# Performance work log

Measured on AMD Instinct MI355X. Metric: run time of the kernel, lower is better.

The kernel has to match this reference:

```python
import jax, jax.numpy as jnp
import numpy as np

NUM_GROUPS = 32
EPS = 1e-6
HEAD = 8


def group_norm(x, gamma, beta):
    # x: (b, c, h, w); normalize per group of channels over (c/g, h, w)
    b, c, h, w = x.shape
    g = NUM_GROUPS
    xg = x.reshape(b, g, c // g, h, w)
    mean = xg.mean(axis=(2, 3, 4), keepdims=True)
    var = xg.var(axis=(2, 3, 4), keepdims=True)
    xn = ((xg - mean) * jax.lax.rsqrt(var + EPS)).reshape(b, c, h, w)
    return xn * gamma[None, :, None, None] + beta[None, :, None, None]


def setup_inputs() -> dict:
    key = jax.random.key(0)
    ks = jax.random.split(key, 6)
    b, c, h, w = 8, 512, 64, 64
    sd = 1.0 / np.sqrt(c)
    return {
        "x": jax.random.normal(ks[0], (b, c, h, w), jnp.float32),
        "gamma": jnp.ones((c,), jnp.float32),
        "beta": jnp.zeros((c,), jnp.float32),
        "Wq": jax.random.normal(ks[1], (c, c), jnp.float32) * sd,
        "Wk": jax.random.normal(ks[2], (c, c), jnp.float32) * sd,
        "Wv": jax.random.normal(ks[3], (c, c), jnp.float32) * sd,
        "Wp": jax.random.normal(ks[4], (c, c), jnp.float32) * sd,
        "bp": jnp.zeros((c,), jnp.float32),
    }


def reference(x, gamma, beta, Wq, Wk, Wv, Wp, bp):
    b, c, h, w = x.shape
    hd = c // HEAD
    scale = jnp.sqrt(jnp.float32(hd))  # NOTE: original MULTIPLIES by sqrt(d)
    xn = group_norm(x, gamma, beta)            # (b, c, h, w)
    x_ = xn.reshape(b, c, h * w).transpose(0, 2, 1)  # (b, n, c), n = h*w
    # torch Linear: y = x @ W.T
    Q = (x_ @ Wq.T).reshape(b, h * w, HEAD, hd)
    K = (x_ @ Wk.T).reshape(b, h * w, HEAD, hd)
    V = (x_ @ Wv.T).reshape(b, h * w, HEAD, hd)
    # einsum 'bhid,bhjd->bhij' with axes (b, n, head, hd): per-position head gram
    dots = jnp.einsum('bnid,bnjd->bnij', Q, K) * scale  # (b, n, head, head)
    att = jax.nn.softmax(dots, axis=1)  # softmax over the SPATIAL axis (dim=1)
    out = jnp.einsum('bnij,bnjd->bnid', att, V).reshape(b, h * w, c)
    out = out @ Wp.T + bp  # dropout is identity at inference
    return out.transpose(0, 2, 1).reshape(b, c, h, w) + xn  # residual adds normed x
```

## Files before the change

kernel.cpp:

```cpp
#include <hip/hip_runtime.h>
#include <stdint.h>

typedef unsigned short ushort_t;
typedef _Float16 half8 __attribute__((ext_vector_type(8)));
typedef float f32x4 __attribute__((ext_vector_type(4)));

#define GLOBAL_AS __attribute__((address_space(1)))
#define LDS_AS    __attribute__((address_space(3)))

__device__ __forceinline__ float bf2f(ushort_t u) {
    union { unsigned i; float f; } v; v.i = ((unsigned)u) << 16; return v.f;
}
__device__ __forceinline__ ushort_t f2h(float f) {
    union { _Float16 h; ushort_t u; } v; v.h = (_Float16)f; return v.u;
}
__device__ __forceinline__ float h2f(ushort_t u) {
    union { _Float16 h; ushort_t u; } v; v.u = u; return (float)v.h;
}

__device__ __forceinline__ void async16(const void* g, void* l) {
    __builtin_amdgcn_global_load_lds((const GLOBAL_AS uint32_t*)g,
                                     (LDS_AS uint32_t*)l, 16, 0, 0);
}

__device__ __forceinline__ int is_bf16_in(const uint32_t* g32) {
    return *g32 == 0x3F803F80u;
}

__global__ __launch_bounds__(256) void prep(const void* Wq, const void* Wk,
                                            const void* Wv, const void* Wp,
                                            const void* g, const void* be, const void* bp,
                                            ushort_t* Wh, float* gcan, float* bcan,
                                            float* bpcan, const uint32_t* g32) {
    const int id = blockIdx.x;
    const int isbf = is_bf16_in(g32);
    if (id < 512) {
        const int wsel = id >> 7, wblk = id & 127;
        const void* src = (wsel == 0) ? Wq : (wsel == 1) ? Wk : (wsel == 2) ? Wv : Wp;
        ushort_t* dst = Wh + (size_t)wsel * 262144;
        const int e0 = wblk * 2048 + threadIdx.x * 8;
        ushort_t o[8];
        if (isbf) {
            uint4 u = *(const uint4*)((const ushort_t*)src + e0);
            const ushort_t* e = (const ushort_t*)&u;
#pragma unroll
            for (int j = 0; j < 8; ++j) o[j] = f2h(bf2f(e[j]));
        } else {
            float4 a = *(const float4*)((const float*)src + e0);
            float4 b = *(const float4*)((const float*)src + e0 + 4);
            o[0] = f2h(a.x); o[1] = f2h(a.y); o[2] = f2h(a.z); o[3] = f2h(a.w);
            o[4] = f2h(b.x); o[5] = f2h(b.y); o[6] = f2h(b.z); o[7] = f2h(b.w);
        }
        *(uint4*)(dst + e0) = *(const uint4*)o;
    } else {
        int t = threadIdx.x + (id - 512) * 256;
        if (isbf) {
            gcan[t]  = bf2f(((const ushort_t*)g)[t]);
            bcan[t]  = bf2f(((const ushort_t*)be)[t]);
            bpcan[t] = bf2f(((const ushort_t*)bp)[t]);
        } else {
            gcan[t]  = ((const float*)g)[t];
            bcan[t]  = ((const float*)be)[t];
            bpcan[t] = ((const float*)bp)[t];
        }
    }
}

__global__ __launch_bounds__(256) void gn_part(const void* xv, float* __restrict__ psums,
                                               const uint32_t* g32) {
    const int bx = blockIdx.x, t = threadIdx.x;
    const size_t base = (size_t)(bx >> 3) * 65536 + (size_t)(bx & 7) * 8192;
    float s = 0.f, sq = 0.f;
    if (is_bf16_in(g32)) {
        const ushort_t* p = (const ushort_t*)xv + base;
        for (int i = 0; i < 4; ++i) {
            uint4 u = ((const uint4*)p)[t + 256 * i];
            const ushort_t* e = (const ushort_t*)&u;
#pragma unroll
            for (int j = 0; j < 8; ++j) { float f = bf2f(e[j]); s += f; sq += f * f; }
        }
    } else {
        const float* p = (const float*)xv + base;
        for (int i = 0; i < 8; ++i) {
            float4 v = ((const float4*)p)[t + 256 * i];
            s += v.x + v.y + v.z + v.w;
            sq += v.x * v.x + v.y * v.y + v.z * v.z + v.w * v.w;
        }
    }
    __shared__ float ls[256], lq[256];
    ls[t] = s; lq[t] = sq;
    __syncthreads();
    for (int off = 128; off > 0; off >>= 1) {
        if (t < off) { ls[t] += ls[t + off]; lq[t] += lq[t + off]; }
        __syncthreads();
    }
    if (t == 0) { psums[bx * 2] = ls[0]; psums[bx * 2 + 1] = lq[0]; }
}

__global__ __launch_bounds__(256) void gn_apply_t(const void* xv,
                                                  const float* __restrict__ gcan,
                                                  const float* __restrict__ bcan,
                                                  const float* __restrict__ psums,
                                                  ushort_t* __restrict__ xnt,
                                                  ushort_t* __restrict__ xnc,
                                                  const uint32_t* g32) {
    const int nt = blockIdx.x;
    const int ct = blockIdx.y;
    const int b  = blockIdx.z;
    const int t  = threadIdx.x;
    const int c0 = ct * 64, n0 = nt * 64;
    __shared__ __align__(16) ushort_t tile[64 * 80];
    __shared__ float scS[64], shS[64];
    if (t < 64) {
        int c = c0 + t;
        int g = c >> 4;
        float s = 0.f, q = 0.f;
#pragma unroll
        for (int k = 0; k < 8; ++k) {
            s += psums[((b * 32 + g) * 8 + k) * 2];
            q += psums[((b * 32 + g) * 8 + k) * 2 + 1];
        }
        float mean = s * (1.f / 65536.f);
        float var  = q * (1.f / 65536.f) - mean * mean;
        float rstd = rsqrtf(fmaxf(var, 0.f) + 1e-6f);
        float sc = rstd * gcan[c];
        scS[t] = sc;
        shS[t] = bcan[c] - mean * sc;
    }
    __syncthreads();
    if (is_bf16_in(g32)) {
        const ushort_t* x = (const ushort_t*)xv;
#pragma unroll
        for (int p = 0; p < 2; ++p) {
            int u = p * 256 + t;
            int cc = u >> 3, nc = u & 7;
            int c = c0 + cc;
            size_t gidx = ((size_t)(b * 512 + c)) * 4096 + n0 + nc * 8;
            uint4 raw = *(const uint4*)(x + gidx);
            float sc = scS[cc], sh = shS[cc];
            const ushort_t* e = (const ushort_t*)&raw;
            ushort_t hv[8];
#pragma unroll
            for (int j = 0; j < 8; ++j) {
                hv[j] = f2h(bf2f(e[j]) * sc + sh);
                tile[(nc * 8 + j) * 80 + cc] = hv[j];
            }
            *(uint4*)(xnc + gidx) = *(const uint4*)hv;
        }
    } else {
        const float* x = (const float*)xv;
#pragma unroll
        for (int p = 0; p < 4; ++p) {
            int u = p * 256 + t;
            int cc = u >> 4, nc = u & 15;
            int c = c0 + cc;
            size_t gidx = ((size_t)(b * 512 + c)) * 4096 + n0 + nc * 4;
            float4 raw = *(const float4*)(x + gidx);
            float sc = scS[cc], sh = shS[cc];
            ushort_t hv[4];
            hv[0] = f2h(raw.x * sc + sh);
            hv[1] = f2h(raw.y * sc + sh);
            hv[2] = f2h(raw.z * sc + sh);
            hv[3] = f2h(raw.w * sc + sh);
#pragma unroll
            for (int j = 0; j < 4; ++j) tile[(nc * 4 + j) * 80 + cc] = hv[j];
            *(uint2*)(xnc + gidx) = *(const uint2*)hv;
        }
    }
    __syncthreads();
#pragma unroll
    for (int p = 0; p < 2; ++p) {
        int u = p * 256 + t;
        int nn = u >> 3, cchunk = u & 7;
        uint4 o = *(const uint4*)(tile + nn * 80 + cchunk * 8);
        *(uint4*)(xnt + ((size_t)(b * 4096 + n0 + nn)) * 512 + c0 + cchunk * 8) = o;
    }
}

__device__ __forceinline__ void gemm256_core(const ushort_t* __restrict__ A,
                                             const ushort_t* __restrict__ Bm,
                                             int m0, int n0, f32x4 acc[8][4]) {
    __shared__ __align__(16) ushort_t lds[2][4][8192];
    const int t = threadIdx.x;
    const int l = t & 63, w = t >> 6;
    const int wmi = w >> 2, wni = w & 3;
    const int lr = l & 15, q = l >> 4;
    const int rxor = lr & 7;
    const int sr = t >> 3;
    const int sc = (t & 7) ^ (sr & 7);

    f32x4 zero = {0.f, 0.f, 0.f, 0.f};
#pragma unroll
    for (int mf = 0; mf < 8; ++mf)
#pragma unroll
        for (int nf = 0; nf < 4; ++nf) acc[mf][nf] = zero;

    auto stage = [&](int kt, int h) {
        const ushort_t* src = ((h < 2) ? A + (size_t)(m0 + h * 128 + sr) * 512
                                       : Bm + (size_t)(n0 + (h - 2) * 128 + sr) * 512)
                              + kt * 64 + sc * 8;
        ushort_t* dst = &lds[kt & 1][h][w * 512];
        async16(src, dst);
        async16(src + 64 * 512, dst + 4096);
    };

    stage(0, 0); stage(0, 1); stage(0, 2); stage(0, 3);
    stage(1, 2); stage(1, 3);
    asm volatile("s_waitcnt vmcnt(4)" ::: "memory");
    __builtin_amdgcn_s_barrier();

    half8 bfr[4][2];
    for (int kt = 0; kt < 8; ++kt) {
        const ushort_t* Ah = &lds[kt & 1][wmi][0];
        const ushort_t* Bh = &lds[kt & 1][2 + (wni >> 1)][(wni & 1) * 4096];
#pragma unroll
        for (int p = 0; p < 4; ++p) {
            half8 afr[2][2];
#pragma unroll
            for (int i = 0; i < 2; ++i)
#pragma unroll
                for (int kh = 0; kh < 2; ++kh)
                    afr[i][kh] = *(const half8*)(Ah + (2 * p + i) * 1024 + lr * 64 +
                                                 (((kh << 2) | q) ^ rxor) * 8);
            if (p == 0) {
#pragma unroll
                for (int nf = 0; nf < 4; ++nf)
#pragma unroll
                    for (int kh = 0; kh < 2; ++kh)
                        bfr[nf][kh] = *(const half8*)(Bh + nf * 1024 + lr * 64 +
                                                      (((kh << 2) | q) ^ rxor) * 8);
            }
            if (p < 2) { if (kt + 1 < 8) stage(kt + 1, p); }
            else       { if (kt + 2 < 8) stage(kt + 2, p); }
            __builtin_amdgcn_s_barrier();
            asm volatile("s_waitcnt lgkmcnt(0)" ::: "memory");
            __builtin_amdgcn_sched_barrier(0);
            __builtin_amdgcn_s_setprio(1);
#pragma unroll
            for (int i = 0; i < 2; ++i)
#pragma unroll
                for (int nf = 0; nf < 4; ++nf) {
                    acc[2 * p + i][nf] = __builtin_amdgcn_mfma_f32_16x16x32_f16(
                        afr[i][0], bfr[nf][0], acc[2 * p + i][nf], 0, 0, 0);
                    acc[2 * p + i][nf] = __builtin_amdgcn_mfma_f32_16x16x32_f16(
                        afr[i][1], bfr[nf][1], acc[2 * p + i][nf], 0, 0, 0);
                }
            __builtin_amdgcn_s_setprio(0);
            __builtin_amdgcn_s_barrier();
        }
        if (kt < 7) {
            if (kt < 6) asm volatile("s_waitcnt vmcnt(4)" ::: "memory");
            else        asm volatile("s_waitcnt vmcnt(0)" ::: "memory");
            __builtin_amdgcn_s_barrier();
        }
    }
}

__global__ __launch_bounds__(512, 2) void gemm_qkv(const ushort_t* __restrict__ xnt,
                                                   const ushort_t* __restrict__ Wh,
                                                   ushort_t* __restrict__ Qo,
                                                   ushort_t* __restrict__ Ko,
                                                   ushort_t* __restrict__ Vo) {
    const int id = blockIdx.x;
    const int xcd = id & 7, s = id >> 3;
    const int mloc = s / 6, r = s % 6;
    const int m0 = (xcd * 16 + mloc) * 256;
    const int n0 = (r & 1) * 256;
    const int z  = r >> 1;
    const ushort_t* B = Wh + (size_t)z * 262144;
    ushort_t* C = (z == 0) ? Qo : (z == 1) ? Ko : Vo;
    f32x4 acc[8][4];
    gemm256_core(xnt, B, m0, n0, acc);
    const int t = threadIdx.x, l = t & 63, w = t >> 6;
    const int wmi = w >> 2, wni = w & 3;
    const int lr = l & 15, q = l >> 4;
#pragma unroll
    for (int mf = 0; mf < 8; ++mf)
#pragma unroll
        for (int nf = 0; nf < 4; ++nf)
#pragma unroll
            for (int rr = 0; rr < 4; ++rr) {
                int row = m0 + wmi * 128 + mf * 16 + q * 4 + rr;
                int cc  = n0 + wni * 64 + nf * 16 + lr;
                C[(size_t)row * 512 + cc] = f2h(acc[mf][nf][rr]);
            }
}

__global__ __launch_bounds__(256) void dots_smax(const ushort_t* __restrict__ Q,
                                                 const ushort_t* __restrict__ K,
                                                 float* __restrict__ dots,
                                                 float* __restrict__ pmax,
                                                 float* __restrict__ psum) {
    const int chunk = blockIdx.x;
    const int t = threadIdx.x, l = t & 63, w = t >> 6;
    const int m = l & 15, q = l >> 4, col = m;
    __shared__ float sd[128][64];
    __shared__ float lm[4][64], lsum[4][64];
#pragma unroll
    for (int i = 0; i < 16; ++i) {
        int gpl = (i * 4 + w) * 2;
        int gp0 = chunk * 128 + gpl;
        const size_t base = (size_t)(gp0 + (m >> 3)) * 512 + (m & 7) * 64 + q * 8;
        half8 a0 = *(const half8*)(Q + base);
        half8 a1 = *(const half8*)(Q + base + 32);
        half8 b0 = *(const half8*)(K + base);
        half8 b1 = *(const half8*)(K + base + 32);
        f32x4 acc = {0.f, 0.f, 0.f, 0.f};
        acc = __builtin_amdgcn_mfma_f32_16x16x32_f16(a0, b0, acc, 0, 0, 0);
        acc = __builtin_amdgcn_mfma_f32_16x16x32_f16(a1, b1, acc, 0, 0, 0);
#pragma unroll
        for (int r = 0; r < 4; ++r) {
            int row = q * 4 + r;
            if (row < 8 && col < 8) {
                float v = acc[r] * 8.0f;
                int ij = row * 8 + col;
                sd[gpl][ij] = v;
                dots[(size_t)(gp0)*64 + ij] = v;
            }
            if (row >= 8 && col >= 8) {
                float v = acc[r] * 8.0f;
                int ij = (row - 8) * 8 + (col - 8);
                sd[gpl + 1][ij] = v;
                dots[(size_t)(gp0 + 1) * 64 + ij] = v;
            }
        }
    }
    __syncthreads();
    const int ij = l;
    float mx = -1e30f;
    float v[32];
#pragma unroll
    for (int r = 0; r < 32; ++r) { v[r] = sd[w * 32 + r][ij]; mx = fmaxf(mx, v[r]); }
    lm[w][ij] = mx;
    __syncthreads();
    float cm = fmaxf(fmaxf(lm[0][ij], lm[1][ij]), fmaxf(lm[2][ij], lm[3][ij]));
    float sum = 0.f;
#pragma unroll
    for (int r = 0; r < 32; ++r) sum += __expf(v[r] - cm);
    lsum[w][ij] = sum;
    __syncthreads();
    if (w == 0) {
        pmax[chunk * 64 + ij] = cm;
        psum[chunk * 64 + ij] = lsum[0][ij] + lsum[1][ij] + lsum[2][ij] + lsum[3][ij];
    }
}

__global__ __launch_bounds__(256) void attn_apply(const float* __restrict__ dots,
                                                  const float* __restrict__ pmax,
                                                  const float* __restrict__ psum,
                                                  const ushort_t* __restrict__ V,
                                                  ushort_t* __restrict__ P) {
    const int t = threadIdx.x, l = t & 63, w = t >> 6;
    const int gp_base = blockIdx.x * 16;
    const int b = gp_base >> 12;
    __shared__ float pm4[4][64], ps4[4][64];
    __shared__ float Mv[64], Siv[64];
    {
        const int cg = w * 8;
        float m = -1e30f;
        float pmv[8], psv[8];
#pragma unroll
        for (int c = 0; c < 8; ++c) {
            pmv[c] = pmax[(b * 32 + cg + c) * 64 + l];
            psv[c] = psum[(b * 32 + cg + c) * 64 + l];
            m = fmaxf(m, pmv[c]);
        }
        float s = 0.f;
#pragma unroll
        for (int c = 0; c < 8; ++c) s += psv[c] * __expf(pmv[c] - m);
        pm4[w][l] = m; ps4[w][l] = s;
    }
    __syncthreads();
    if (w == 0) {
        float M = fmaxf(fmaxf(pm4[0][l], pm4[1][l]), fmaxf(pm4[2][l], pm4[3][l]));
        float S = ps4[0][l] * __expf(pm4[0][l] - M) + ps4[1][l] * __expf(pm4[1][l] - M)
                + ps4[2][l] * __expf(pm4[2][l] - M) + ps4[3][l] * __expf(pm4[3][l] - M);
        Mv[l] = M;
        Siv[l] = 1.f / S;
    }
    __syncthreads();
    const float mv = Mv[l], siv = Siv[l];
    __shared__ float att[4][64];
    __shared__ __align__(16) ushort_t vb[4][512];
    const int i = l >> 3, dc = l & 7;
    for (int p = 0; p < 4; ++p) {
        int gp = gp_base + w * 4 + p;
        float d = dots[(size_t)gp * 64 + l];
        att[w][l] = __expf(d - mv) * siv;
        *(uint4*)(&vb[w][l * 8]) = *(const uint4*)(V + (size_t)gp * 512 + l * 8);
        float o[8] = {0, 0, 0, 0, 0, 0, 0, 0};
#pragma unroll
        for (int j = 0; j < 8; ++j) {
            float a = att[w][i * 8 + j];
            uint4 vv = *(const uint4*)(&vb[w][j * 64 + dc * 8]);
            const ushort_t* ve = (const ushort_t*)&vv;
#pragma unroll
            for (int k2 = 0; k2 < 8; ++k2) o[k2] += a * h2f(ve[k2]);
        }
        ushort_t ou[8];
#pragma unroll
        for (int k2 = 0; k2 < 8; ++k2) ou[k2] = f2h(o[k2]);
        *(uint4*)(P + (size_t)gp * 512 + l * 8) = *(const uint4*)ou;
    }
}

__global__ __launch_bounds__(512, 2) void gemm_out(const ushort_t* __restrict__ Wph,
                                                   const ushort_t* __restrict__ P,
                                                   const ushort_t* __restrict__ xnc,
                                                   const float* __restrict__ bpcan,
                                                   float* __restrict__ out) {
    const int id = blockIdx.x;
    const int b  = id & 7;
    const int s  = id >> 3;
    const int o0 = (s & 1) * 256;
    const int n1 = (s >> 1) * 256;
    f32x4 acc[8][4];
    gemm256_core(Wph, P + (size_t)b * 4096 * 512, o0, n1, acc);
    const int t = threadIdx.x, l = t & 63, w = t >> 6;
    const int wmi = w >> 2, wni = w & 3;
    const int lr = l & 15, q = l >> 4;
#pragma unroll
    for (int mf = 0; mf < 8; ++mf) {
#pragma unroll
        for (int rr = 0; rr < 4; ++rr) {
            int o = o0 + wmi * 128 + mf * 16 + q * 4 + rr;
            float bias = bpcan[o];
#pragma unroll
            for (int nf = 0; nf < 4; ++nf) {
                int n = n1 + wni * 64 + nf * 16 + lr;
                size_t idx = ((size_t)(b * 512 + o)) * 4096 + n;
                out[idx] = acc[mf][nf][rr] + bias + h2f(xnc[idx]);
            }
        }
    }
}

extern "C" void kernel_launch(void* const* d_in, const int* in_sizes, int n_in,
                              void* d_out, int out_size, void* d_ws, size_t ws_size,
                              hipStream_t stream) {
    const void* x     = d_in[0];
    const void* gamma = d_in[1];
    const void* beta  = d_in[2];
    const void* Wq    = d_in[3];
    const void* Wk    = d_in[4];
    const void* Wv    = d_in[5];
    const void* Wp    = d_in[6];
    const void* bp    = d_in[7];
    const uint32_t* g32 = (const uint32_t*)gamma;
    float* out = (float*)d_out;

    char* ws = (char*)d_ws;
    const size_t SZ = 33554432;
    ushort_t* xnt = (ushort_t*)(ws);
    ushort_t* Qh  = (ushort_t*)(ws + 1 * SZ);
    ushort_t* Kh  = (ushort_t*)(ws + 2 * SZ);
    ushort_t* Vh  = (ushort_t*)(ws + 3 * SZ);
    float* dots   = (float*)(ws + 4 * SZ);
    ushort_t* Wh  = (ushort_t*)(ws + 4 * SZ + 8388608);
    ushort_t* xnc = (ushort_t*)(ws + 4 * SZ + 8388608 + 2097152);
    char* tail    = ws + 4 * SZ + 8388608 + 2097152 + SZ;
    float* gcan   = (float*)(tail);
    float* bcan   = gcan + 512;
    float* bpcan  = bcan + 512;
    float* psums  = bpcan + 512;
    float* pmax   = psums + 4096;
    float* psumS  = pmax + 16384;
    ushort_t* Pb  = xnt;

    prep      <<<514, 256, 0, stream>>>(Wq, Wk, Wv, Wp, gamma, beta, bp,
                                        Wh, gcan, bcan, bpcan, g32);
    gn_part   <<<2048, 256, 0, stream>>>(x, psums, g32);
    gn_apply_t<<<dim3(64, 8, 8), 256, 0, stream>>>(x, gcan, bcan, psums, xnt, xnc, g32);
    gemm_qkv  <<<768, 512, 0, stream>>>(xnt, Wh, Qh, Kh, Vh);
    dots_smax <<<256, 256, 0, stream>>>(Qh, Kh, dots, pmax, psumS);
    attn_apply<<<2048, 256, 0, stream>>>(dots, pmax, psumS, Vh, Pb);
    gemm_out  <<<256, 512, 0, stream>>>(Wh + 3 * 262144, Pb, xnc, bpcan, out);
}
```

Measured before the change: 267.8 us.

## Software-pipeline LDS fragment loads against MFMA in QKV GEMM core

Restructures the GEMM inner loop so A fragments for the next sub-tile are read from LDS while the current sub-tile's MFMAs run, using double-buffered register fragments (cur/nxt). Global and LDS address arithmetic is precomputed outside the loop into base pointers. Each phase now has one barrier instead of two, which shortens sync time. The cost is higher register pressure from the extra fragment buffers, and there is some risk around the ordering of barriers against the async stage writes.

```diff
diff --git a/kernel.cpp b/kernel.cpp
--- a/kernel.cpp
+++ b/kernel.cpp
@@ -22,6 +22,9 @@
     __builtin_amdgcn_global_load_lds((const GLOBAL_AS uint32_t*)g,
                                      (LDS_AS uint32_t*)l, 16, 0, 0);
 }
+
+#define LGKM0_SB do { asm volatile("s_waitcnt lgkmcnt(0)" ::: "memory"); \
+                      __builtin_amdgcn_sched_barrier(0); } while (0)
 
 __device__ __forceinline__ int is_bf16_in(const uint32_t* g32) {
     return *g32 == 0x3F803F80u;
@@ -189,68 +192,126 @@
     const int sr = t >> 3;
     const int sc = (t & 7) ^ (sr & 7);
 
+    const ushort_t* gA0 = A  + (size_t)(m0 + sr) * 512 + sc * 8;
+    const ushort_t* gA1 = A  + (size_t)(m0 + 128 + sr) * 512 + sc * 8;
+    const ushort_t* gB0 = Bm + (size_t)(n0 + sr) * 512 + sc * 8;
+    const ushort_t* gB1 = Bm + (size_t)(n0 + 128 + sr) * 512 + sc * 8;
+
+    const int cK0 = (q ^ rxor) * 8;
+    const int cK1 = ((4 | q) ^ rxor) * 8;
+    const ushort_t* lbase = &lds[0][0][0];
+    const ushort_t* pA0 = lbase + wmi * 8192 + lr * 64 + cK0;
+    const ushort_t* pA1 = lbase + wmi * 8192 + lr * 64 + cK1;
+    const ushort_t* pB0 = lbase + (2 + (wni >> 1)) * 8192 + (wni & 1) * 4096 + lr * 64 + cK0;
+    const ushort_t* pB1 = lbase + (2 + (wni >> 1)) * 8192 + (wni & 1) * 4096 + lr * 64 + cK1;
+
+    auto stg = [&](const ushort_t* gp, int kt, int h) {
+        ushort_t* d = (ushort_t*)(&lds[0][0][0]) + (kt & 1) * 32768 + h * 8192 + w * 512;
+        async16(gp + kt * 64, d);
+        async16(gp + kt * 64 + 64 * 512, d + 4096);
+    };
+
     f32x4 zero = {0.f, 0.f, 0.f, 0.f};
 #pragma unroll
     for (int mf = 0; mf < 8; ++mf)
 #pragma unroll
         for (int nf = 0; nf < 4; ++nf) acc[mf][nf] = zero;
 
-    auto stage = [&](int kt, int h) {
-        const ushort_t* src = ((h < 2) ? A + (size_t)(m0 + h * 128 + sr) * 512
-                                       : Bm + (size_t)(n0 + (h - 2) * 128 + sr) * 512)
-                              + kt * 64 + sc * 8;
-        ushort_t* dst = &lds[kt & 1][h][w * 512];
-        async16(src, dst);
-        async16(src + 64 * 512, dst + 4096);
-    };
-
-    stage(0, 0); stage(0, 1); stage(0, 2); stage(0, 3);
-    stage(1, 2); stage(1, 3);
+    stg(gA0, 0, 0); stg(gA1, 0, 1); stg(gB0, 0, 2); stg(gB1, 0, 3);
+    stg(gB0, 1, 2); stg(gB1, 1, 3);
     asm volatile("s_waitcnt vmcnt(4)" ::: "memory");
     __builtin_amdgcn_s_barrier();
 
-    half8 bfr[4][2];
     for (int kt = 0; kt < 8; ++kt) {
-        const ushort_t* Ah = &lds[kt & 1][wmi][0];
-        const ushort_t* Bh = &lds[kt & 1][2 + (wni >> 1)][(wni & 1) * 4096];
-#pragma unroll
-        for (int p = 0; p < 4; ++p) {
-            half8 afr[2][2];
-#pragma unroll
-            for (int i = 0; i < 2; ++i)
-#pragma unroll
-                for (int kh = 0; kh < 2; ++kh)
-                    afr[i][kh] = *(const half8*)(Ah + (2 * p + i) * 1024 + lr * 64 +
-                                                 (((kh << 2) | q) ^ rxor) * 8);
-            if (p == 0) {
-#pragma unroll
-                for (int nf = 0; nf < 4; ++nf)
-#pragma unroll
-                    for (int kh = 0; kh < 2; ++kh)
-                        bfr[nf][kh] = *(const half8*)(Bh + nf * 1024 + lr * 64 +
-                                                      (((kh << 2) | q) ^ rxor) * 8);
-            }
-            if (p < 2) { if (kt + 1 < 8) stage(kt + 1, p); }
-            else       { if (kt + 2 < 8) stage(kt + 2, p); }
-            __builtin_amdgcn_s_barrier();
-            asm volatile("s_waitcnt lgkmcnt(0)" ::: "memory");
-            __builtin_amdgcn_sched_barrier(0);
-            __builtin_amdgcn_s_setprio(1);
-#pragma unroll
-            for (int i = 0; i < 2; ++i)
-#pragma unroll
-                for (int nf = 0; nf < 4; ++nf) {
-                    acc[2 * p + i][nf] = __builtin_amdgcn_mfma_f32_16x16x32_f16(
-                        afr[i][0], bfr[nf][0], acc[2 * p + i][nf], 0, 0, 0);
-                    acc[2 * p + i][nf] = __builtin_amdgcn_mfma_f32_16x16x32_f16(
-                        afr[i][1], bfr[nf][1], acc[2 * p + i][nf], 0, 0, 0);
-                }
-            __builtin_amdgcn_s_setprio(0);
-            __builtin_amdgcn_s_barrier();
-        }
-        if (kt < 7) {
-            if (kt < 6) asm volatile("s_waitcnt vmcnt(4)" ::: "memory");
-            else        asm volatile("s_waitcnt vmcnt(0)" ::: "memory");
+        const int bo = (kt & 1) << 15;
+        const ushort_t* a0 = pA0 + bo;
+        const ushort_t* a1 = pA1 + bo;
+        const ushort_t* b0 = pB0 + bo;
+        const ushort_t* b1 = pB1 + bo;
+        half8 bfr[4][2], cur[2][2], nxt[2][2];
+#pragma unroll
+        for (int nf = 0; nf < 4; ++nf) {
+            bfr[nf][0] = *(const half8*)(b0 + nf * 1024);
+            bfr[nf][1] = *(const half8*)(b1 + nf * 1024);
+        }
+#pragma unroll
+        for (int i = 0; i < 2; ++i) {
+            cur[i][0] = *(const half8*)(a0 + i * 1024);
+            cur[i][1] = *(const half8*)(a1 + i * 1024);
+        }
+        if (kt + 1 < 8) stg(gA0, kt + 1, 0);
+        LGKM0_SB;
+#pragma unroll
+        for (int i = 0; i < 2; ++i) {
+            nxt[i][0] = *(const half8*)(a0 + (2 + i) * 1024);
+            nxt[i][1] = *(const half8*)(a1 + (2 + i) * 1024);
+        }
+        if (kt + 1 < 8) stg(gA1, kt + 1, 1);
+        __builtin_amdgcn_s_setprio(1);
+#pragma unroll
+        for (int i = 0; i < 2; ++i)
+#pragma unroll
+            for (int nf = 0; nf < 4; ++nf) {
+                acc[i][nf] = __builtin_amdgcn_mfma_f32_16x16x32_f16(
+                    cur[i][0], bfr[nf][0], acc[i][nf], 0, 0, 0);
+                acc[i][nf] = __builtin_amdgcn_mfma_f32_16x16x32_f16(
+                    cur[i][1], bfr[nf][1], acc[i][nf], 0, 0, 0);
+            }
+        __builtin_amdgcn_s_setprio(0);
+        __builtin_amdgcn_s_barrier();
+        LGKM0_SB;
+#pragma unroll
+        for (int i = 0; i < 2; ++i) {
+            cur[i][0] = *(const half8*)(a0 + (4 + i) * 1024);
+            cur[i][1] = *(const half8*)(a1 + (4 + i) * 1024);
+        }
+        if (kt + 2 < 8) stg(gB0, kt + 2, 2);
+        __builtin_amdgcn_s_setprio(1);
+#pragma unroll
+        for (int i = 0; i < 2; ++i)
+#pragma unroll
+            for (int nf = 0; nf < 4; ++nf) {
+                acc[2 + i][nf] = __builtin_amdgcn_mfma_f32_16x16x32_f16(
+                    nxt[i][0], bfr[nf][0], acc[2 + i][nf], 0, 0, 0);
+                acc[2 + i][nf] = __builtin_amdgcn_mfma_f32_16x16x32_f16(
+                    nxt[i][1], bfr[nf][1], acc[2 + i][nf], 0, 0, 0);
+            }
+        __builtin_amdgcn_s_setprio(0);
+        __builtin_amdgcn_s_barrier();
+        LGKM0_SB;
+#pragma unroll
+        for (int i = 0; i < 2; ++i) {
+            nxt[i][0] = *(const half8*)(a0 + (6 + i) * 1024);
+            nxt[i][1] = *(const half8*)(a1 + (6 + i) * 1024);
+        }
+        if (kt + 2 < 8) stg(gB1, kt + 2, 3);
+        __builtin_amdgcn_s_setprio(1);
+#pragma unroll
+        for (int i = 0; i < 2; ++i)
+#pragma unroll
+            for (int nf = 0; nf < 4; ++nf) {
+                acc[4 + i][nf] = __builtin_amdgcn_mfma_f32_16x16x32_f16(
+                    cur[i][0], bfr[nf][0], acc[4 + i][nf], 0, 0, 0);
+                acc[4 + i][nf] = __builtin_amdgcn_mfma_f32_16x16x32_f16(
+                    cur[i][1], bfr[nf][1], acc[4 + i][nf], 0, 0, 0);
+            }
+        __builtin_amdgcn_s_setprio(0);
+        __builtin_amdgcn_s_barrier();
+        LGKM0_SB;
+        __builtin_amdgcn_s_setprio(1);
+#pragma unroll
+        for (int i = 0; i < 2; ++i)
+#pragma unroll
+            for (int nf = 0; nf < 4; ++nf) {
+                acc[6 + i][nf] = __builtin_amdgcn_mfma_f32_16x16x32_f16(
+                    nxt[i][0], bfr[nf][0], acc[6 + i][nf], 0, 0, 0);
+                acc[6 + i][nf] = __builtin_amdgcn_mfma_f32_16x16x32_f16(
+                    nxt[i][1], bfr[nf][1], acc[6 + i][nf], 0, 0, 0);
+            }
+        __builtin_amdgcn_s_setprio(0);
+        if (kt + 1 < 8) {
+            if (kt + 2 < 8) asm volatile("s_waitcnt vmcnt(4)" ::: "memory");
+            else            asm volatile("s_waitcnt vmcnt(0)" ::: "memory");
             __builtin_amdgcn_s_barrier();
         }
     }
```

New measurement: 271.3 us. No clear change (+1.3%).

## Load GEMM weight fragments directly from global into registers, halving LDS staging

Applied to the files above, without the earlier changes.

The 256x256 GEMM core no longer stages the weight (B) tile through LDS. Each wave now loads its B fragments straight from global memory into double-buffered registers (even/odd sets) one k-tile ahead, and only A is staged asynchronously into a smaller LDS buffer. This halves LDS footprint and LDS read traffic and removes the B staging step, but adds register pressure and direct global loads of weight rows that several waves read redundantly (mostly served by cache). The k-loop is also restructured with macros into four phases per tile.

```diff
diff --git a/kernel.cpp b/kernel.cpp
--- a/kernel.cpp
+++ b/kernel.cpp
@@ -177,10 +177,68 @@
     }
 }
 
+#define GPHASE(S0, S1, BU, EXTRA)                                              \
+    {                                                                          \
+        half8 x00 = *(const half8*)(a0 + (S0) * 1024);                         \
+        half8 x01 = *(const half8*)(a1 + (S0) * 1024);                         \
+        half8 x10 = *(const half8*)(a0 + (S1) * 1024);                         \
+        half8 x11 = *(const half8*)(a1 + (S1) * 1024);                         \
+        EXTRA                                                                  \
+        __builtin_amdgcn_s_barrier();                                          \
+        asm volatile("s_waitcnt lgkmcnt(0)" ::: "memory");                     \
+        __builtin_amdgcn_sched_barrier(0);                                     \
+        __builtin_amdgcn_s_setprio(1);                                         \
+        _Pragma("unroll")                                                      \
+        for (int nf = 0; nf < 4; ++nf) {                                       \
+            acc[(S0)][nf] = __builtin_amdgcn_mfma_f32_16x16x32_f16(            \
+                x00, BU[nf][0], acc[(S0)][nf], 0, 0, 0);                       \
+            acc[(S0)][nf] = __builtin_amdgcn_mfma_f32_16x16x32_f16(            \
+                x01, BU[nf][1], acc[(S0)][nf], 0, 0, 0);                       \
+            acc[(S1)][nf] = __builtin_amdgcn_mfma_f32_16x16x32_f16(            \
+                x10, BU[nf][0], acc[(S1)][nf], 0, 0, 0);                       \
+            acc[(S1)][nf] = __builtin_amdgcn_mfma_f32_16x16x32_f16(            \
+                x11, BU[nf][1], acc[(S1)][nf], 0, 0, 0);                       \
+        }                                                                      \
+        __builtin_amdgcn_s_setprio(0);                                         \
+    }
+
+#define GTILE(KT, BU, BF)                                                      \
+    {                                                                          \
+        const ushort_t* a0 = pA0 + (((KT) & 1) << 14);                         \
+        const ushort_t* a1 = pA1 + (((KT) & 1) << 14);                         \
+        const bool more = (KT) + 1 < 8;                                        \
+        const int ktn = ((KT) + 1) * 64;                                       \
+        GPHASE(0, 1, BU,                                                       \
+            if (more) {                                                        \
+                stgA(gA0, (KT) + 1, 0);                                        \
+                BF[0][0] = *(const half8*)(gB + 0 * 8192 + 0 * 32 + ktn);      \
+                BF[0][1] = *(const half8*)(gB + 0 * 8192 + 1 * 32 + ktn);      \
+                BF[1][0] = *(const half8*)(gB + 1 * 8192 + 0 * 32 + ktn);      \
+                BF[1][1] = *(const half8*)(gB + 1 * 8192 + 1 * 32 + ktn);      \
+            })                                                                 \
+        __builtin_amdgcn_s_barrier();                                          \
+        GPHASE(2, 3, BU,                                                       \
+            if (more) {                                                        \
+                stgA(gA1, (KT) + 1, 1);                                        \
+                BF[2][0] = *(const half8*)(gB + 2 * 8192 + 0 * 32 + ktn);      \
+                BF[2][1] = *(const half8*)(gB + 2 * 8192 + 1 * 32 + ktn);      \
+                BF[3][0] = *(const half8*)(gB + 3 * 8192 + 0 * 32 + ktn);      \
+                BF[3][1] = *(const half8*)(gB + 3 * 8192 + 1 * 32 + ktn);      \
+            })                                                                 \
+        __builtin_amdgcn_s_barrier();                                          \
+        GPHASE(4, 5, BU, )                                                     \
+        __builtin_amdgcn_s_barrier();                                          \
+        GPHASE(6, 7, BU, )                                                     \
+        if (more) {                                                            \
+            asm volatile("s_waitcnt vmcnt(0)" ::: "memory");                   \
+            __builtin_amdgcn_s_barrier();                                      \
+        }                                                                      \
+    }
+
 __device__ __forceinline__ void gemm256_core(const ushort_t* __restrict__ A,
                                              const ushort_t* __restrict__ Bm,
                                              int m0, int n0, f32x4 acc[8][4]) {
-    __shared__ __align__(16) ushort_t lds[2][4][8192];
+    __shared__ __align__(16) ushort_t lds[2][2][8192];
     const int t = threadIdx.x;
     const int l = t & 63, w = t >> 6;
     const int wmi = w >> 2, wni = w & 3;
@@ -189,70 +247,42 @@
     const int sr = t >> 3;
     const int sc = (t & 7) ^ (sr & 7);
 
+    const ushort_t* gA0 = A + (size_t)(m0 + sr) * 512 + sc * 8;
+    const ushort_t* gA1 = A + (size_t)(m0 + 128 + sr) * 512 + sc * 8;
+    const ushort_t* gB = Bm + (size_t)(n0 + wni * 64 + lr) * 512 + q * 8;
+
+    const int cK0 = (q ^ rxor) * 8;
+    const int cK1 = ((4 | q) ^ rxor) * 8;
+    ushort_t* lbase = &lds[0][0][0];
+    const ushort_t* pA0 = lbase + wmi * 8192 + lr * 64 + cK0;
+    const ushort_t* pA1 = lbase + wmi * 8192 + lr * 64 + cK1;
+
+    auto stgA = [&](const ushort_t* gp, int kt, int h) {
+        ushort_t* d = lbase + ((kt & 1) << 14) + (h << 13) + w * 512;
+        async16(gp + kt * 64, d);
+        async16(gp + kt * 64 + 64 * 512, d + 4096);
+    };
+
     f32x4 zero = {0.f, 0.f, 0.f, 0.f};
 #pragma unroll
     for (int mf = 0; mf < 8; ++mf)
 #pragma unroll
         for (int nf = 0; nf < 4; ++nf) acc[mf][nf] = zero;
 
-    auto stage = [&](int kt, int h) {
-        const ushort_t* src = ((h < 2) ? A + (size_t)(m0 + h * 128 + sr) * 512
-                                       : Bm + (size_t)(n0 + (h - 2) * 128 + sr) * 512)
-                              + kt * 64 + sc * 8;
-        ushort_t* dst = &lds[kt & 1][h][w * 512];
-        async16(src, dst);
-        async16(src + 64 * 512, dst + 4096);
-    };
-
-    stage(0, 0); stage(0, 1); stage(0, 2); stage(0, 3);
-    stage(1, 2); stage(1, 3);
-    asm volatile("s_waitcnt vmcnt(4)" ::: "memory");
+    half8 bfrE[4][2], bfrO[4][2];
+
+    stgA(gA0, 0, 0); stgA(gA1, 0, 1);
+#pragma unroll
+    for (int nf = 0; nf < 4; ++nf) {
+        bfrE[nf][0] = *(const half8*)(gB + nf * 8192 + 0 * 32);
+        bfrE[nf][1] = *(const half8*)(gB + nf * 8192 + 1 * 32);
+    }
+    asm volatile("s_waitcnt vmcnt(0)" ::: "memory");
     __builtin_amdgcn_s_barrier();
 
-    half8 bfr[4][2];
-    for (int kt = 0; kt < 8; ++kt) {
-        const ushort_t* Ah = &lds[kt & 1][wmi][0];
-        const ushort_t* Bh = &lds[kt & 1][2 + (wni >> 1)][(wni & 1) * 4096];
-#pragma unroll
-        for (int p = 0; p < 4; ++p) {
-            half8 afr[2][2];
-#pragma unroll
-            for (int i = 0; i < 2; ++i)
-#pragma unroll
-                for (int kh = 0; kh < 2; ++kh)
-                    afr[i][kh] = *(const half8*)(Ah + (2 * p + i) * 1024 + lr * 64 +
-                                                 (((kh << 2) | q) ^ rxor) * 8);
-            if (p == 0) {
-#pragma unroll
-                for (int nf = 0; nf < 4; ++nf)
-#pragma unroll
-                    for (int kh = 0; kh < 2; ++kh)
-                        bfr[nf][kh] = *(const half8*)(Bh + nf * 1024 + lr * 64 +
-                                                      (((kh << 2) | q) ^ rxor) * 8);
-            }
-            if (p < 2) { if (kt + 1 < 8) stage(kt + 1, p); }
-            else       { if (kt + 2 < 8) stage(kt + 2, p); }
-            __builtin_amdgcn_s_barrier();
-            asm volatile("s_waitcnt lgkmcnt(0)" ::: "memory");
-            __builtin_amdgcn_sched_barrier(0);
-            __builtin_amdgcn_s_setprio(1);
-#pragma unroll
-            for (int i = 0; i < 2; ++i)
-#pragma unroll
-                for (int nf = 0; nf < 4; ++nf) {
-                    acc[2 * p + i][nf] = __builtin_amdgcn_mfma_f32_16x16x32_f16(
-                        afr[i][0], bfr[nf][0], acc[2 * p + i][nf], 0, 0, 0);
-                    acc[2 * p + i][nf] = __builtin_amdgcn_mfma_f32_16x16x32_f16(
-                        afr[i][1], bfr[nf][1], acc[2 * p + i][nf], 0, 0, 0);
-                }
-            __builtin_amdgcn_s_setprio(0);
-            __builtin_amdgcn_s_barrier();
-        }
-        if (kt < 7) {
-            if (kt < 6) asm volatile("s_waitcnt vmcnt(4)" ::: "memory");
-            else        asm volatile("s_waitcnt vmcnt(0)" ::: "memory");
-            __builtin_amdgcn_s_barrier();
-        }
+    for (int kt2 = 0; kt2 < 8; kt2 += 2) {
+        GTILE(kt2, bfrE, bfrO)
+        GTILE(kt2 + 1, bfrO, bfrE)
     }
 }
 
```

After: 308.5 us. +15.2%, slower.
